# Kernel tuning notes

Measured on AMD Instinct MI355X. Metric: run time of the kernel, lower is better.

Reference implementation:

```python
import jax, jax.numpy as jnp
import numpy as np

QLEN, BSZ, D_MODEL = 1024, 4, 1024
N_HEAD, D_HEAD = 16, 64
NEG = -1e30


def _layer_norm(x, g, b, eps=1e-5):
    mu = jnp.mean(x, axis=-1, keepdims=True)
    var = jnp.mean((x - mu) ** 2, axis=-1, keepdims=True)
    return (x - mu) / jnp.sqrt(var + eps) * g + b


def _rel_shift(x):
    # x: [qlen, klen, bsz, n_head] -- Transformer-XL relative shift
    q, k, b, n = x.shape
    x = jnp.pad(x, ((0, 0), (1, 0), (0, 0), (0, 0)))  # zero-pad along klen front
    x = x.reshape(k + 1, q, b, n)[1:]
    return x.reshape(q, k, b, n)


def setup_inputs() -> dict:
    key = jax.random.key(0)
    ks = jax.random.split(key, 8)
    s = 0.02
    w = jax.random.normal(ks[0], (QLEN, BSZ, D_MODEL), jnp.float32)
    r = jax.random.normal(ks[1], (QLEN, D_MODEL), jnp.float32)
    r_w_bias = jax.random.normal(ks[2], (N_HEAD, D_HEAD), jnp.float32) * s
    r_r_bias = jax.random.normal(ks[3], (N_HEAD, D_HEAD), jnp.float32) * s
    attn_mask = jnp.tril(jnp.ones((QLEN, QLEN), dtype=bool))  # causal: True = attend
    W_qkv = jax.random.normal(ks[4], (D_MODEL, 3 * N_HEAD * D_HEAD), jnp.float32) * s
    W_r = jax.random.normal(ks[5], (D_MODEL, N_HEAD * D_HEAD), jnp.float32) * s
    W_o = jax.random.normal(ks[6], (N_HEAD * D_HEAD, D_MODEL), jnp.float32) * s
    gamma = jnp.ones((D_MODEL,), jnp.float32)
    beta = jnp.zeros((D_MODEL,), jnp.float32)
    return {"w": w, "r": r, "r_w_bias": r_w_bias, "r_r_bias": r_r_bias,
            "attn_mask": attn_mask, "W_qkv": W_qkv, "W_r": W_r, "W_o": W_o,
            "gamma": gamma, "beta": beta}


def reference(w, r, r_w_bias, r_r_bias, attn_mask, W_qkv, W_r, W_o, gamma, beta):
    qlen, bsz, _ = w.shape
    scale = 1.0 / (D_HEAD ** 0.5)
    heads = w @ W_qkv                                    # [q, b, 3*n*d]
    q_h, k_h, v_h = jnp.split(heads, 3, axis=-1)
    q_h = q_h.reshape(qlen, bsz, N_HEAD, D_HEAD)
    k_h = k_h.reshape(qlen, bsz, N_HEAD, D_HEAD)
    v_h = v_h.reshape(qlen, bsz, N_HEAD, D_HEAD)
    r_k = (r @ W_r).reshape(-1, N_HEAD, D_HEAD)          # [rlen, n, d]
    AC = jnp.einsum('ibnd,jbnd->ijbn', q_h + r_w_bias, k_h)
    BD = jnp.einsum('ibnd,jnd->ijbn', q_h + r_r_bias, r_k)
    BD = _rel_shift(BD)
    score = (AC + BD) * scale                            # [q, k, b, n]
    score = jnp.where(attn_mask[:, :, None, None], score, NEG)
    prob = jax.nn.softmax(score, axis=1)
    vec = jnp.einsum('ijbn,jbnd->ibnd', prob, v_h).reshape(qlen, bsz, N_HEAD * D_HEAD)
    attn_out = vec @ W_o
    return _layer_norm(w + attn_out, gamma, beta)
```

## Files before the change

### kernel.cpp

```cpp
#include <hip/hip_runtime.h>
#include <math.h>

constexpr int QLEN_C  = 1024;
constexpr int BSZ_C   = 4;
constexpr int DMODEL  = 1024;
constexpr float SCALE = 0.125f;
constexpr float NEGF  = -1e30f;

typedef __attribute__((ext_vector_type(8))) short bh8;
typedef __attribute__((ext_vector_type(4))) float f32x4;

__device__ inline short f2bf(float f) {
    union { float f; unsigned u; } v; v.f = f;
    unsigned r = v.u + 0x7FFFu + ((v.u >> 16) & 1u);
    return (short)(r >> 16);
}
__device__ inline float bf2f(short s) {
    union { unsigned u; float f; } v;
    v.u = ((unsigned)(unsigned short)s) << 16;
    return v.f;
}
__device__ inline void gload16(const void* g, void* l) {
    __builtin_amdgcn_global_load_lds(
        (__attribute__((address_space(1))) void*)g,
        (__attribute__((address_space(3))) void*)l, 16, 0, 0);
}
__device__ inline void wave_lds_fence() {
    __builtin_amdgcn_sched_barrier(0);
    __builtin_amdgcn_s_waitcnt(0xC07F);
    __builtin_amdgcn_sched_barrier(0);
}

__global__ __launch_bounds__(256)
void gemm12_fused(const short* __restrict__ wb, const short* __restrict__ WqkvT,
                  short* __restrict__ headsb,
                  const short* __restrict__ rb, const short* __restrict__ WrT,
                  short* __restrict__ rkb)
{
    constexpr int BK = 32;
    constexpr int K  = 1024;
    __shared__ alignas(16) short As[128 * BK];
    __shared__ alignas(16) short Bs[128 * BK];

    const int bid = blockIdx.x;
    const short* A;  const short* BT;  short* C;  int N;
    int bx, by;
    if (bid < 768) {
        A = wb;  BT = WqkvT;  C = headsb;  N = 3072;
        bx = bid % 24;  by = bid / 24;
    } else {
        A = rb;  BT = WrT;    C = rkb;     N = 1024;
        int t = bid - 768;  bx = t & 7;  by = t >> 3;
    }

    const int tid = threadIdx.x;
    const int wave = tid >> 6, lane = tid & 63;
    const int quad = lane >> 4, c = lane & 15;
    const int wr = wave >> 1, wc = wave & 1;
    const int row0 = by * 128, col0 = bx * 128;

    const int ch0 = wave * 128 + lane, ch1 = ch0 + 64;
    const int m0 = ch0 >> 2, s0 = ch0 & 3;
    const int m1 = ch1 >> 2, s1 = ch1 & 3;

    f32x4 acc[4][4];
    #pragma unroll
    for (int i = 0; i < 4; ++i)
        #pragma unroll
        for (int j = 0; j < 4; ++j) acc[i][j] = (f32x4)0.0f;

    for (int k0 = 0; k0 < K; k0 += BK) {
        gload16(A  + (size_t)(row0 + m0) * K + k0 + s0 * 8, (char*)As + ch0 * 16);
        gload16(A  + (size_t)(row0 + m1) * K + k0 + s1 * 8, (char*)As + ch1 * 16);
        gload16(BT + (size_t)(col0 + m0) * K + k0 + s0 * 8, (char*)Bs + ch0 * 16);
        gload16(BT + (size_t)(col0 + m1) * K + k0 + s1 * 8, (char*)Bs + ch1 * 16);
        __syncthreads();

        bh8 aF[4], bF[4];
        #pragma unroll
        for (int mi = 0; mi < 4; ++mi)
            aF[mi] = *(const bh8*)&As[(wr * 64 + mi * 16 + c) * BK + quad * 8];
        #pragma unroll
        for (int ni = 0; ni < 4; ++ni)
            bF[ni] = *(const bh8*)&Bs[(wc * 64 + ni * 16 + c) * BK + quad * 8];
        #pragma unroll
        for (int mi = 0; mi < 4; ++mi)
            #pragma unroll
            for (int ni = 0; ni < 4; ++ni)
                acc[mi][ni] = __builtin_amdgcn_mfma_f32_16x16x32_bf16(
                    aF[mi], bF[ni], acc[mi][ni], 0, 0, 0);
        __syncthreads();
    }

    #pragma unroll
    for (int mi = 0; mi < 4; ++mi)
        #pragma unroll
        for (int ni = 0; ni < 4; ++ni)
            #pragma unroll
            for (int r = 0; r < 4; ++r) {
                int orow = row0 + wr * 64 + mi * 16 + quad * 4 + r;
                int ocol = col0 + wc * 64 + ni * 16 + c;
                ((short*)C)[(size_t)orow * N + ocol] = f2bf(acc[mi][ni][r]);
            }
}

__global__ __launch_bounds__(256)
void gemm_wo_sk(const short* __restrict__ A, const short* __restrict__ BT,
                float* __restrict__ C0, float* __restrict__ C1)
{
    constexpr int BK = 32;
    constexpr int N  = 1024, K = 1024;
    __shared__ alignas(16) short As[128 * BK];
    __shared__ alignas(16) short Bs[128 * BK];

    const int bid = blockIdx.x;
    const int half = bid & 1, tile = bid >> 1;
    const int bx = tile & 7, by = tile >> 3;
    const int k_lo = half * 512;
    float* C = half ? C1 : C0;

    const int tid = threadIdx.x;
    const int wave = tid >> 6, lane = tid & 63;
    const int quad = lane >> 4, c = lane & 15;
    const int wr = wave >> 1, wc = wave & 1;
    const int row0 = by * 128, col0 = bx * 128;

    const int ch0 = wave * 128 + lane, ch1 = ch0 + 64;
    const int m0 = ch0 >> 2, s0 = ch0 & 3;
    const int m1 = ch1 >> 2, s1 = ch1 & 3;

    f32x4 acc[4][4];
    #pragma unroll
    for (int i = 0; i < 4; ++i)
        #pragma unroll
        for (int j = 0; j < 4; ++j) acc[i][j] = (f32x4)0.0f;

    for (int k0 = k_lo; k0 < k_lo + 512; k0 += BK) {
        gload16(A  + (size_t)(row0 + m0) * K + k0 + s0 * 8, (char*)As + ch0 * 16);
        gload16(A  + (size_t)(row0 + m1) * K + k0 + s1 * 8, (char*)As + ch1 * 16);
        gload16(BT + (size_t)(col0 + m0) * K + k0 + s0 * 8, (char*)Bs + ch0 * 16);
        gload16(BT + (size_t)(col0 + m1) * K + k0 + s1 * 8, (char*)Bs + ch1 * 16);
        __syncthreads();

        bh8 aF[4], bF[4];
        #pragma unroll
        for (int mi = 0; mi < 4; ++mi)
            aF[mi] = *(const bh8*)&As[(wr * 64 + mi * 16 + c) * BK + quad * 8];
        #pragma unroll
        for (int ni = 0; ni < 4; ++ni)
            bF[ni] = *(const bh8*)&Bs[(wc * 64 + ni * 16 + c) * BK + quad * 8];
        #pragma unroll
        for (int mi = 0; mi < 4; ++mi)
            #pragma unroll
            for (int ni = 0; ni < 4; ++ni)
                acc[mi][ni] = __builtin_amdgcn_mfma_f32_16x16x32_bf16(
                    aF[mi], bF[ni], acc[mi][ni], 0, 0, 0);
        __syncthreads();
    }

    #pragma unroll
    for (int mi = 0; mi < 4; ++mi)
        #pragma unroll
        for (int ni = 0; ni < 4; ++ni)
            #pragma unroll
            for (int r = 0; r < 4; ++r) {
                int orow = row0 + wr * 64 + mi * 16 + quad * 4 + r;
                int ocol = col0 + wc * 64 + ni * 16 + c;
                C[(size_t)orow * N + ocol] = acc[mi][ni][r];
            }
}

__device__ inline void transp_tile(const float* __restrict__ B, short* __restrict__ BT,
                                   int K, int N, int n0, int k0, int t,
                                   float (*tile)[68])
{
    const int row = t >> 2, c4 = t & 3;
    const float* src = B + (size_t)(k0 + row) * N + n0 + c4 * 16;
    #pragma unroll
    for (int u = 0; u < 4; ++u) {
        float4 v = *(const float4*)(src + u * 4);
        tile[row][c4 * 16 + u * 4 + 0] = v.x;
        tile[row][c4 * 16 + u * 4 + 1] = v.y;
        tile[row][c4 * 16 + u * 4 + 2] = v.z;
        tile[row][c4 * 16 + u * 4 + 3] = v.w;
    }
    __syncthreads();
    const int nl = t >> 2, kc = t & 3;
    short tmp[16];
    #pragma unroll
    for (int e = 0; e < 16; ++e) tmp[e] = f2bf(tile[kc * 16 + e][nl]);
    short* dst = BT + (size_t)(n0 + nl) * K + k0 + kc * 16;
    *(bh8*)dst = *(bh8*)&tmp[0];
    *(bh8*)(dst + 8) = *(bh8*)&tmp[8];
}

__global__ __launch_bounds__(256)
void prep_all(const float* __restrict__ w, const float* __restrict__ r,
              const float* __restrict__ Wqkv, const float* __restrict__ Wr,
              const float* __restrict__ Wo,
              short* __restrict__ wb, short* __restrict__ rb,
              short* __restrict__ WqkvT, short* __restrict__ WrT,
              short* __restrict__ WoT, short* __restrict__ rkb)
{
    __shared__ float tile[64][68];
    const int bid = blockIdx.x;
    const int t = threadIdx.x;

    if (bid < 2048) {
        int idx = (bid * 256 + t) * 8;
        bh8 o;
        #pragma unroll
        for (int e = 0; e < 8; ++e) o[e] = f2bf(w[idx + e]);
        *(bh8*)(wb + idx) = o;
    } else if (bid < 2560) {
        int idx = ((bid - 2048) * 256 + t) * 8;
        bh8 o;
        #pragma unroll
        for (int e = 0; e < 8; ++e) o[e] = f2bf(r[idx + e]);
        *(bh8*)(rb + idx) = o;
    } else if (bid < 3328) {
        int tt = bid - 2560;
        transp_tile(Wqkv, WqkvT, 1024, 3072, (tt % 48) * 64, (tt / 48) * 64, t, tile);
    } else if (bid < 3584) {
        int tt = bid - 3328;
        transp_tile(Wr, WrT, 1024, 1024, (tt % 16) * 64, (tt / 16) * 64, t, tile);
    } else if (bid < 3840) {
        int tt = bid - 3584;
        transp_tile(Wo, WoT, 1024, 1024, (tt % 16) * 64, (tt / 16) * 64, t, tile);
    } else {
        int idx = 1024 * 1024 + ((bid - 3840) * 256 + t) * 8;
        bh8 z;
        #pragma unroll
        for (int e = 0; e < 8; ++e) z[e] = 0;
        *(bh8*)(rkb + idx) = z;
    }
}

__global__ __launch_bounds__(256)
void prep_kv2(const short* __restrict__ headsb, const short* __restrict__ rkb,
              short* __restrict__ kfrag, short* __restrict__ vfrag,
              short* __restrict__ rfrag)
{
    __shared__ short vtile[64][72];
    const int blk = blockIdx.x;
    const int t = threadIdx.x;

    if (blk < 1024) {
        const int bn = blk >> 4, ju = blk & 15;
        const int b = bn & 3, nn = bn >> 2;
        const int j0 = ju * 64;
        const int row = t >> 2, d0 = (t & 3) * 16;

        const short* kp = headsb + ((size_t)(j0 + row) * 4 + b) * 3072 + 1024 + nn * 64 + d0;
        const short* vp = kp + 1024;
        bh8 k0 = *(const bh8*)kp, k1 = *(const bh8*)(kp + 8);
        bh8 v0 = *(const bh8*)vp, v1 = *(const bh8*)(vp + 8);

        {
            const int jtile = (j0 + row) >> 4, cc = row & 15;
            short* kb_bn = kfrag + (size_t)bn * 65536 + (size_t)jtile * 1024 + cc * 8;
            const int d1 = d0 + 8;
            *(bh8*)(kb_bn + (d0 >> 5) * 512 + ((d0 >> 3) & 3) * 128) = k0;
            *(bh8*)(kb_bn + (d1 >> 5) * 512 + ((d1 >> 3) & 3) * 128) = k1;
        }
        #pragma unroll
        for (int e = 0; e < 8; ++e) {
            vtile[row][d0 + e] = v0[e];
            vtile[row][d0 + 8 + e] = v1[e];
        }
        __syncthreads();
        const int d = t >> 2, jl0 = (t & 3) * 16;
        short tmp[16];
        #pragma unroll
        for (int e = 0; e < 16; ++e) tmp[e] = vtile[jl0 + e][d];
        short* vb = vfrag + (size_t)bn * 65536 + (size_t)ju * 4096
                  + (d >> 4) * 1024 + (d & 15) * 8;
        const int jl1 = jl0 + 8;
        *(bh8*)(vb + (jl0 >> 5) * 512 + ((jl0 >> 3) & 3) * 128) = *(bh8*)&tmp[0];
        *(bh8*)(vb + (jl1 >> 5) * 512 + ((jl1 >> 3) & 3) * 128) = *(bh8*)&tmp[8];
    } else {
        const int rblk = blk - 1024;
        const int row = rblk * 4 + (t >> 6);
        const int col0 = (t & 63) * 16;
        const short* src = rkb + (size_t)row * 1024 + col0;
        bh8 r0 = *(const bh8*)src, r1 = *(const bh8*)(src + 8);
        const int rt = row >> 4, cc = row & 15;
        const int nn = col0 >> 6, dd = col0 & 63, dd1 = dd + 8;
        short* dst = rfrag + (size_t)rt * 16384 + nn * 1024 + cc * 8;
        *(bh8*)(dst + (dd  >> 5) * 512 + ((dd  >> 3) & 3) * 128) = r0;
        *(bh8*)(dst + (dd1 >> 5) * 512 + ((dd1 >> 3) & 3) * 128) = r1;
    }
}

__global__ __launch_bounds__(256)
void attn_mfma(const short* __restrict__ headsb, const short* __restrict__ rfrag,
               const short* __restrict__ kfrag, const short* __restrict__ vfrag,
               const float* __restrict__ rwb, const float* __restrict__ rrb,
               short* __restrict__ vecb)
{
    __shared__ alignas(16) short sP[4][2][16 * 80];

    const int tid = threadIdx.x;
    const int wave = tid >> 6, lane = tid & 63;
    const int quad = lane >> 4, c = lane & 15;

    const int bi = blockIdx.x;
    const int itile = 15 - (bi >> 6);
    const int bn = bi & 63;
    const int n = bn >> 2, b = bn & 3;
    const int nU = itile + 1;
    const int rb = itile * 64 + wave * 16;

    const int dq = n * 64 + quad * 8;
    const short* kbp = kfrag + (size_t)bn * 65536;
    const short* vtp = vfrag + (size_t)bn * 65536;
    const int lin = quad * 128 + c * 8;

    bh8 ones;
    #pragma unroll
    for (int e = 0; e < 8; ++e) ones[e] = (short)0x3F80;

    bh8 aAC[2], aBD[2];
    #pragma unroll
    for (int ks = 0; ks < 2; ++ks) {
        const short* qp = headsb + ((size_t)(rb + c) * 4 + b) * 3072 + dq + 32 * ks;
        bh8 q8 = *(const bh8*)qp;
        #pragma unroll
        for (int e = 0; e < 8; ++e) {
            float qv = bf2f(q8[e]);
            aAC[ks][e] = f2bf(qv + rwb[dq + 32 * ks + e]);
            aBD[ks][e] = f2bf(qv + rrb[dq + 32 * ks + e]);
        }
    }

    bh8 rkv[10], kbv[8];
    auto pf = [&](int j0) {
        const int rt0 = (1008 - rb + j0) >> 4;
        #pragma unroll
        for (int tt = 0; tt < 5; ++tt) {
            const short* rp = rfrag + (size_t)(rt0 + tt) * 16384 + n * 1024 + lin;
            rkv[2 * tt]     = *(const bh8*)rp;
            rkv[2 * tt + 1] = *(const bh8*)(rp + 512);
        }
        const int jt0 = j0 >> 4;
        #pragma unroll
        for (int jt = 0; jt < 4; ++jt) {
            const short* kp = kbp + (size_t)(jt0 + jt) * 1024 + lin;
            kbv[2 * jt]     = *(const bh8*)kp;
            kbv[2 * jt + 1] = *(const bh8*)(kp + 512);
        }
    };

    f32x4 oacc[4], lacc;
    float m_r[4];
    #pragma unroll
    for (int dt = 0; dt < 4; ++dt) oacc[dt] = (f32x4)0.0f;
    lacc = (f32x4)0.0f;
    #pragma unroll
    for (int r = 0; r < 4; ++r) m_r[r] = -3.0e38f;

    pf(0);
    int j0 = 0;

    for (int u = 0; u < nU; ++u) {
        short* PL = &sP[wave][u & 1][0];

        bh8 vvv[8];
        {
            const short* vup = vtp + (size_t)(j0 >> 6) * 4096;
            #pragma unroll
            for (int dt = 0; dt < 4; ++dt) {
                const short* vp = vup + dt * 1024 + lin;
                vvv[2 * dt]     = *(const bh8*)vp;
                vvv[2 * dt + 1] = *(const bh8*)(vp + 512);
            }
        }

        f32x4 bt[5];
        #pragma unroll
        for (int tt = 0; tt < 5; ++tt) {
            bt[tt] = (f32x4)0.0f;
            bt[tt] = __builtin_amdgcn_mfma_f32_16x16x32_bf16(aBD[0], rkv[2 * tt], bt[tt], 0, 0, 0);
            bt[tt] = __builtin_amdgcn_mfma_f32_16x16x32_bf16(aBD[1], rkv[2 * tt + 1], bt[tt], 0, 0, 0);
        }
        f32x4 ac[4];
        #pragma unroll
        for (int jt = 0; jt < 4; ++jt) {
            ac[jt] = (f32x4)0.0f;
            ac[jt] = __builtin_amdgcn_mfma_f32_16x16x32_bf16(aAC[0], kbv[2 * jt], ac[jt], 0, 0, 0);
            ac[jt] = __builtin_amdgcn_mfma_f32_16x16x32_bf16(aAC[1], kbv[2 * jt + 1], ac[jt], 0, 0, 0);
        }

        if (u + 1 < nU) pf(j0 + 64);

        float al[4];
        #pragma unroll
        for (int r = 0; r < 4; ++r) {
            const int row = quad * 4 + r;
            const int o = 15 - row;
            const int src = (lane & 48) | ((c + o) & 15);
            const int gi = rb + row;
            float s[4];
            float mx = -3.0e38f;
            #pragma unroll
            for (int jt = 0; jt < 4; ++jt) {
                float sval = (c < o) ? bt[jt + 1][r] : bt[jt][r];
                float bd = __shfl(sval, src, 64);
                int gj = j0 + c + 16 * jt;
                float v = SCALE * (ac[jt][r] + bd);
                if (gj > gi) v = NEGF;
                s[jt] = v;
                mx = fmaxf(mx, v);
            }
            #pragma unroll
            for (int msk = 1; msk < 16; msk <<= 1)
                mx = fmaxf(mx, __shfl_xor(mx, msk, 64));
            float mnew = fmaxf(m_r[r], mx);
            al[r] = __expf(m_r[r] - mnew);
            m_r[r] = mnew;
            #pragma unroll
            for (int jt = 0; jt < 4; ++jt)
                PL[row * 80 + c + 16 * jt] = f2bf(__expf(s[jt] - mnew));
            #pragma unroll
            for (int dt = 0; dt < 4; ++dt) oacc[dt][r] *= al[r];
            lacc[r] *= al[r];
        }

        wave_lds_fence();

        bh8 aP[2];
        #pragma unroll
        for (int ks = 0; ks < 2; ++ks)
            aP[ks] = *(const bh8*)(PL + c * 80 + 32 * ks + quad * 8);
        #pragma unroll
        for (int dt = 0; dt < 4; ++dt) {
            oacc[dt] = __builtin_amdgcn_mfma_f32_16x16x32_bf16(aP[0], vvv[2 * dt], oacc[dt], 0, 0, 0);
            oacc[dt] = __builtin_amdgcn_mfma_f32_16x16x32_bf16(aP[1], vvv[2 * dt + 1], oacc[dt], 0, 0, 0);
        }
        lacc = __builtin_amdgcn_mfma_f32_16x16x32_bf16(aP[0], ones, lacc, 0, 0, 0);
        lacc = __builtin_amdgcn_mfma_f32_16x16x32_bf16(aP[1], ones, lacc, 0, 0, 0);

        j0 += 64;
    }

    #pragma unroll
    for (int r = 0; r < 4; ++r) {
        float rinv = 1.f / lacc[r];
        int gi = rb + quad * 4 + r;
        short* op = vecb + ((size_t)gi * 4 + b) * 1024 + n * 64;
        #pragma unroll
        for (int dt = 0; dt < 4; ++dt)
            op[c + 16 * dt] = f2bf(oacc[dt][r] * rinv);
    }
}

__global__ __launch_bounds__(256)
void ln_kernel(const float* __restrict__ w, const float* __restrict__ a0,
               const float* __restrict__ a1,
               const float* __restrict__ gamma, const float* __restrict__ beta,
               float* __restrict__ out)
{
    const int row = blockIdx.x;
    const int tid = threadIdx.x;
    const float4* xw4 = (const float4*)(w  + (size_t)row * DMODEL);
    const float4* p04 = (const float4*)(a0 + (size_t)row * DMODEL);
    const float4* p14 = (const float4*)(a1 + (size_t)row * DMODEL);

    float4 a = xw4[tid], b0 = p04[tid], b1 = p14[tid];
    float x[4] = {a.x + b0.x + b1.x, a.y + b0.y + b1.y,
                  a.z + b0.z + b1.z, a.w + b0.w + b1.w};
    float s = x[0] + x[1] + x[2] + x[3];

    __shared__ float red[6];
    #pragma unroll
    for (int m = 1; m < 64; m <<= 1) s += __shfl_xor(s, m, 64);
    int wv = tid >> 6, lnid = tid & 63;
    if (lnid == 0) red[wv] = s;
    __syncthreads();
    if (tid == 0) red[4] = red[0] + red[1] + red[2] + red[3];
    __syncthreads();
    float mu = red[4] * (1.f / DMODEL);

    float vs = 0.f;
    #pragma unroll
    for (int e = 0; e < 4; ++e) { float d = x[e] - mu; vs += d * d; }
    #pragma unroll
    for (int m = 1; m < 64; m <<= 1) vs += __shfl_xor(vs, m, 64);
    if (lnid == 0) red[wv] = vs;
    __syncthreads();
    if (tid == 0) red[5] = red[0] + red[1] + red[2] + red[3];
    __syncthreads();
    float var = red[5] * (1.f / DMODEL);
    float inv = rsqrtf(var + 1e-5f);

    float4 g = ((const float4*)gamma)[tid];
    float4 be = ((const float4*)beta)[tid];
    float4 o;
    o.x = (x[0] - mu) * inv * g.x + be.x;
    o.y = (x[1] - mu) * inv * g.y + be.y;
    o.z = (x[2] - mu) * inv * g.z + be.z;
    o.w = (x[3] - mu) * inv * g.w + be.w;
    ((float4*)(out + (size_t)row * DMODEL))[tid] = o;
}

extern "C" void kernel_launch(void* const* d_in, const int* in_sizes, int n_in,
                              void* d_out, int out_size, void* d_ws, size_t ws_size,
                              hipStream_t stream)
{
    const float* w     = (const float*)d_in[0];
    const float* r     = (const float*)d_in[1];
    const float* rwb   = (const float*)d_in[2];
    const float* rrb   = (const float*)d_in[3];
    const float* Wqkv  = (const float*)d_in[5];
    const float* Wr    = (const float*)d_in[6];
    const float* Wo    = (const float*)d_in[7];
    const float* gamma = (const float*)d_in[8];
    const float* beta  = (const float*)d_in[9];
    float* out = (float*)d_out;

    short* headsb = (short*)d_ws;
    short* wb     = headsb + 12582912;
    short* WqkvT  = wb + 4194304;
    short* rb     = WqkvT + 3145728;
    short* WrT    = rb + 1048576;
    short* WoT    = WrT + 1048576;
    short* rkb    = WoT + 1048576;
    short* kfrag  = rkb + 1114112;
    short* vfrag  = kfrag + 4194304;
    short* vecb   = vfrag + 4194304;

    short* rfrag  = rb;

    float* attno0 = (float*)headsb;
    float* attno1 = (float*)wb;

    prep_all<<<3872, 256, 0, stream>>>(w, r, Wqkv, Wr, Wo, wb, rb, WqkvT, WrT, WoT, rkb);
    gemm12_fused<<<dim3(832), 256, 0, stream>>>(wb, WqkvT, headsb, rb, WrT, rkb);
    prep_kv2<<<dim3(1296), 256, 0, stream>>>(headsb, rkb, kfrag, vfrag, rfrag);
    attn_mfma<<<dim3(1024), 256, 0, stream>>>(headsb, rfrag, kfrag, vfrag, rwb, rrb, vecb);
    gemm_wo_sk<<<dim3(512), 256, 0, stream>>>(vecb, WoT, attno0, attno1);
    ln_kernel<<<4096, 256, 0, stream>>>(w, attno0, attno1, gamma, beta, out);
}
```

Baseline: 149.1 us.

## Rewrite QKV/R projection GEMM with 256x256 tiles and double-buffered async prefetch

Replaces the 128x128, BK=32, single-buffered fused projection GEMM with a 512-thread kernel that computes 256x256 tiles at BK=64. Global-to-LDS loads are double-buffered and interleaved between MFMA groups, with explicit vmcnt waits and raised wave priority. Output now goes through LDS so each thread writes 16-byte vectors to global memory. The aim is to hide load latency and raise operand reuse. The trade-off is only 208 blocks, which may under-fill the GPU, plus higher register and LDS pressure.

```diff
diff --git a/kernel.cpp b/kernel.cpp
--- a/kernel.cpp
+++ b/kernel.cpp
@@ -30,78 +30,174 @@
     __builtin_amdgcn_s_waitcnt(0xC07F);
     __builtin_amdgcn_sched_barrier(0);
 }
-
-__global__ __launch_bounds__(256)
-void gemm12_fused(const short* __restrict__ wb, const short* __restrict__ WqkvT,
-                  short* __restrict__ headsb,
-                  const short* __restrict__ rb, const short* __restrict__ WrT,
-                  short* __restrict__ rkb)
-{
-    constexpr int BK = 32;
-    constexpr int K  = 1024;
-    __shared__ alignas(16) short As[128 * BK];
-    __shared__ alignas(16) short Bs[128 * BK];
+__device__ inline void block_sync() {
+    __builtin_amdgcn_sched_barrier(0);
+    __builtin_amdgcn_s_barrier();
+    __builtin_amdgcn_sched_barrier(0);
+}
+__device__ inline void wait_vm8() {
+    __builtin_amdgcn_sched_barrier(0);
+    asm volatile("s_waitcnt vmcnt(8)" ::: "memory");
+    __builtin_amdgcn_sched_barrier(0);
+}
+__device__ inline void wait_vm0() {
+    __builtin_amdgcn_sched_barrier(0);
+    asm volatile("s_waitcnt vmcnt(0)" ::: "memory");
+    __builtin_amdgcn_sched_barrier(0);
+}
+
+__global__ __launch_bounds__(512, 2)
+void gemm12_8ph(const short* __restrict__ wb, const short* __restrict__ WqkvT,
+                short* __restrict__ headsb,
+                const short* __restrict__ rb, const short* __restrict__ WrT,
+                short* __restrict__ rkb)
+{
+    constexpr int NT = 16;
+    __shared__ alignas(16) short Ald[2][2][128][64];
+    __shared__ alignas(16) short Bld[2][2][128][64];
 
     const int bid = blockIdx.x;
-    const short* A;  const short* BT;  short* C;  int N;
-    int bx, by;
-    if (bid < 768) {
-        A = wb;  BT = WqkvT;  C = headsb;  N = 3072;
-        bx = bid % 24;  by = bid / 24;
+    const short* A; const short* BT; short* Cc; int Nn; int bx, by;
+    if (bid < 192) {
+        A = wb; BT = WqkvT; Cc = headsb; Nn = 3072;
+        bx = bid % 12; by = bid / 12;
     } else {
-        A = rb;  BT = WrT;    C = rkb;     N = 1024;
-        int t = bid - 768;  bx = t & 7;  by = t >> 3;
-    }
+        int q = bid - 192;
+        A = rb; BT = WrT; Cc = rkb; Nn = 1024;
+        bx = q & 3; by = q >> 2;
+    }
+    const int row0 = by * 256, col0 = bx * 256;
 
     const int tid = threadIdx.x;
-    const int wave = tid >> 6, lane = tid & 63;
+    const int wid = tid >> 6, lane = tid & 63;
     const int quad = lane >> 4, c = lane & 15;
-    const int wr = wave >> 1, wc = wave & 1;
-    const int row0 = by * 128, col0 = bx * 128;
-
-    const int ch0 = wave * 128 + lane, ch1 = ch0 + 64;
-    const int m0 = ch0 >> 2, s0 = ch0 & 3;
-    const int m1 = ch1 >> 2, s1 = ch1 & 3;
-
-    f32x4 acc[4][4];
-    #pragma unroll
-    for (int i = 0; i < 4; ++i)
-        #pragma unroll
-        for (int j = 0; j < 4; ++j) acc[i][j] = (f32x4)0.0f;
-
-    for (int k0 = 0; k0 < K; k0 += BK) {
-        gload16(A  + (size_t)(row0 + m0) * K + k0 + s0 * 8, (char*)As + ch0 * 16);
-        gload16(A  + (size_t)(row0 + m1) * K + k0 + s1 * 8, (char*)As + ch1 * 16);
-        gload16(BT + (size_t)(col0 + m0) * K + k0 + s0 * 8, (char*)Bs + ch0 * 16);
-        gload16(BT + (size_t)(col0 + m1) * K + k0 + s1 * 8, (char*)Bs + ch1 * 16);
-        __syncthreads();
-
-        bh8 aF[4], bF[4];
-        #pragma unroll
-        for (int mi = 0; mi < 4; ++mi)
-            aF[mi] = *(const bh8*)&As[(wr * 64 + mi * 16 + c) * BK + quad * 8];
-        #pragma unroll
-        for (int ni = 0; ni < 4; ++ni)
-            bF[ni] = *(const bh8*)&Bs[(wc * 64 + ni * 16 + c) * BK + quad * 8];
-        #pragma unroll
-        for (int mi = 0; mi < 4; ++mi)
-            #pragma unroll
-            for (int ni = 0; ni < 4; ++ni)
-                acc[mi][ni] = __builtin_amdgcn_mfma_f32_16x16x32_bf16(
-                    aF[mi], bF[ni], acc[mi][ni], 0, 0, 0);
-        __syncthreads();
-    }
-
-    #pragma unroll
-    for (int mi = 0; mi < 4; ++mi)
-        #pragma unroll
-        for (int ni = 0; ni < 4; ++ni)
-            #pragma unroll
-            for (int r = 0; r < 4; ++r) {
-                int orow = row0 + wr * 64 + mi * 16 + quad * 4 + r;
-                int ocol = col0 + wc * 64 + ni * 16 + c;
-                ((short*)C)[(size_t)orow * N + ocol] = f2bf(acc[mi][ni][r]);
+    const int wr = wid >> 2, wcn = wid & 3;
+    const int hb = wcn >> 1;
+
+    auto stage_half = [&](short* dst, const short* src, int srcRow0, int kcol) {
+        gload16(src + (size_t)(srcRow0 + (tid >> 3)) * 1024 + kcol + (tid & 7) * 8,
+                (char*)dst + tid * 16);
+        const int t2 = tid + 512;
+        gload16(src + (size_t)(srcRow0 + (t2 >> 3)) * 1024 + kcol + (t2 & 7) * 8,
+                (char*)dst + t2 * 16);
+    };
+
+    f32x4 acc[8][4];
+    #pragma unroll
+    for (int mf = 0; mf < 8; ++mf)
+        #pragma unroll
+        for (int nf = 0; nf < 4; ++nf) acc[mf][nf] = (f32x4)0.0f;
+
+    stage_half(&Ald[0][0][0][0], A, row0,        0);
+    stage_half(&Ald[0][1][0][0], A, row0 + 128,  0);
+    stage_half(&Bld[0][0][0][0], BT, col0,       0);
+    stage_half(&Bld[0][1][0][0], BT, col0 + 128, 0);
+    stage_half(&Ald[1][0][0][0], A, row0,        64);
+    stage_half(&Ald[1][1][0][0], A, row0 + 128,  64);
+    stage_half(&Bld[1][0][0][0], BT, col0,       64);
+    stage_half(&Bld[1][1][0][0], BT, col0 + 128, 64);
+    wait_vm8();
+    block_sync();
+
+    for (int t = 0; t < NT; ++t) {
+        const int d = t & 1;
+
+        bh8 aF[8][2], bF[4][2];
+        #pragma unroll
+        for (int mf = 0; mf < 8; ++mf)
+            #pragma unroll
+            for (int ks = 0; ks < 2; ++ks)
+                aF[mf][ks] = *(const bh8*)&Ald[d][wr][mf * 16 + c][ks * 32 + quad * 8];
+        #pragma unroll
+        for (int nf = 0; nf < 4; ++nf)
+            #pragma unroll
+            for (int ks = 0; ks < 2; ++ks)
+                bF[nf][ks] = *(const bh8*)&Bld[d][hb][(wcn & 1) * 64 + nf * 16 + c][ks * 32 + quad * 8];
+
+        wave_lds_fence();
+        block_sync();
+
+        const int ts = t + 2;
+
+        __builtin_amdgcn_s_setprio(1);
+        #pragma unroll
+        for (int mf = 0; mf < 4; ++mf)
+            #pragma unroll
+            for (int nf = 0; nf < 2; ++nf) {
+                acc[mf][nf] = __builtin_amdgcn_mfma_f32_16x16x32_bf16(aF[mf][0], bF[nf][0], acc[mf][nf], 0, 0, 0);
+                acc[mf][nf] = __builtin_amdgcn_mfma_f32_16x16x32_bf16(aF[mf][1], bF[nf][1], acc[mf][nf], 0, 0, 0);
             }
+        __builtin_amdgcn_s_setprio(0);
+
+        if (ts < NT) {
+            stage_half(&Ald[d][0][0][0], A, row0,       ts * 64);
+            stage_half(&Ald[d][1][0][0], A, row0 + 128, ts * 64);
+        }
+
+        __builtin_amdgcn_s_setprio(1);
+        #pragma unroll
+        for (int mf = 0; mf < 4; ++mf)
+            #pragma unroll
+            for (int nf = 2; nf < 4; ++nf) {
+                acc[mf][nf] = __builtin_amdgcn_mfma_f32_16x16x32_bf16(aF[mf][0], bF[nf][0], acc[mf][nf], 0, 0, 0);
+                acc[mf][nf] = __builtin_amdgcn_mfma_f32_16x16x32_bf16(aF[mf][1], bF[nf][1], acc[mf][nf], 0, 0, 0);
+            }
+        __builtin_amdgcn_s_setprio(0);
+
+        if (ts < NT) {
+            stage_half(&Bld[d][0][0][0], BT, col0,       ts * 64);
+            stage_half(&Bld[d][1][0][0], BT, col0 + 128, ts * 64);
+        }
+
+        __builtin_amdgcn_s_setprio(1);
+        #pragma unroll
+        for (int mf = 4; mf < 8; ++mf)
+            #pragma unroll
+            for (int nf = 0; nf < 2; ++nf) {
+                acc[mf][nf] = __builtin_amdgcn_mfma_f32_16x16x32_bf16(aF[mf][0], bF[nf][0], acc[mf][nf], 0, 0, 0);
+                acc[mf][nf] = __builtin_amdgcn_mfma_f32_16x16x32_bf16(aF[mf][1], bF[nf][1], acc[mf][nf], 0, 0, 0);
+            }
+        #pragma unroll
+        for (int mf = 4; mf < 8; ++mf)
+            #pragma unroll
+            for (int nf = 2; nf < 4; ++nf) {
+                acc[mf][nf] = __builtin_amdgcn_mfma_f32_16x16x32_bf16(aF[mf][0], bF[nf][0], acc[mf][nf], 0, 0, 0);
+                acc[mf][nf] = __builtin_amdgcn_mfma_f32_16x16x32_bf16(aF[mf][1], bF[nf][1], acc[mf][nf], 0, 0, 0);
+            }
+        __builtin_amdgcn_s_setprio(0);
+
+        if (t + 2 < NT)      wait_vm8();
+        else if (t + 1 < NT) wait_vm0();
+        if (t + 1 < NT)      block_sync();
+    }
+
+    wave_lds_fence();
+    block_sync();
+    short* cst = &Ald[0][0][0][0];
+    const int crow = tid >> 2, cseg = tid & 3;
+    #pragma unroll
+    for (int pass = 0; pass < 2; ++pass) {
+        if (wr == pass) {
+            #pragma unroll
+            for (int mf = 0; mf < 8; ++mf)
+                #pragma unroll
+                for (int nf = 0; nf < 4; ++nf)
+                    #pragma unroll
+                    for (int rr = 0; rr < 4; ++rr)
+                        cst[(mf * 16 + quad * 4 + rr) * 256 + wcn * 64 + nf * 16 + c] =
+                            f2bf(acc[mf][nf][rr]);
+        }
+        wave_lds_fence();
+        block_sync();
+        {
+            short* gp = Cc + (size_t)(row0 + pass * 128 + crow) * Nn + col0 + cseg * 64;
+            const short* lp = &cst[crow * 256 + cseg * 64];
+            #pragma unroll
+            for (int u = 0; u < 8; ++u)
+                *(bh8*)(gp + u * 8) = *(const bh8*)(lp + u * 8);
+        }
+        if (pass == 0) { wave_lds_fence(); block_sync(); }
+    }
 }
 
 __global__ __launch_bounds__(256)
@@ -535,7 +631,7 @@
     float* attno1 = (float*)wb;
 
     prep_all<<<3872, 256, 0, stream>>>(w, r, Wqkv, Wr, Wo, wb, rb, WqkvT, WrT, WoT, rkb);
-    gemm12_fused<<<dim3(832), 256, 0, stream>>>(wb, WqkvT, headsb, rb, WrT, rkb);
+    gemm12_8ph<<<dim3(208), 512, 0, stream>>>(wb, WqkvT, headsb, rb, WrT, rkb);
     prep_kv2<<<dim3(1296), 256, 0, stream>>>(headsb, rkb, kfrag, vfrag, rfrag);
     attn_mfma<<<dim3(1024), 256, 0, stream>>>(headsb, rfrag, kfrag, vfrag, rwb, rrb, vecb);
     gemm_wo_sk<<<dim3(512), 256, 0, stream>>>(vecb, WoT, attno0, attno1);
```

Result: no change. 149.8 us (+0.5%).
